# Optimization experiments

Hardware: AMD Instinct MI355X
Metric: run time of the kernel (lower is better)

The kernel has to match this reference:

```python
import jax, jax.numpy as jnp
import numpy as np

V, FC = 6890, 13776
N, H, W, K = 2, 336, 336, 28
SIGMA, GAMMA, EPS = 1e-4, 1e-4, 1e-10
ZNEAR, ZFAR = 1.0, 100.0
SHININESS = 64.0
BG = jnp.array([1.0, 1.0, 1.0], jnp.float32)


def setup_inputs() -> dict:
    key = jax.random.key(0)
    ks = jax.random.split(key, 10)
    verts = jax.random.normal(ks[0], (V, 3), jnp.float32)
    vert_colors = jax.random.uniform(ks[1], (V, 3), jnp.float32)
    faces = jax.random.randint(ks[2], (FC, 3), 0, V)
    # shift so ~1/FC entries are -1 (background), as in PyTorch3D Fragments
    pix_to_face = jax.random.randint(ks[3], (N, H, W, K), 0, FC + 1) - 1
    u = jax.random.uniform(ks[4], (N, H, W, K, 3), jnp.float32) + 1e-3
    bary_coords = u / u.sum(-1, keepdims=True)
    dists = jax.random.normal(ks[5], (N, H, W, K), jnp.float32) * 1e-4
    zbuf = jnp.sort(jax.random.uniform(ks[6], (N, H, W, K), jnp.float32) * 10.0 + 2.0, axis=-1)
    light_location = jnp.array([0.0, 0.0, 10.0], jnp.float32)
    ambient_color = jnp.full((3,), 0.5, jnp.float32)
    diffuse_color = jnp.full((3,), 0.3, jnp.float32)
    specular_color = jnp.full((3,), 0.2, jnp.float32)
    camera_position = jnp.array([0.0, 0.0, 2.7], jnp.float32)
    return dict(verts=verts, vert_colors=vert_colors, faces=faces,
                pix_to_face=pix_to_face, bary_coords=bary_coords, dists=dists,
                zbuf=zbuf, light_location=light_location,
                ambient_color=ambient_color, diffuse_color=diffuse_color,
                specular_color=specular_color, camera_position=camera_position)


def _normalize(x, eps=1e-6):
    return x / jnp.maximum(jnp.linalg.norm(x, axis=-1, keepdims=True), eps)


def reference(verts, vert_colors, faces, pix_to_face, bary_coords, dists, zbuf,
              light_location, ambient_color, diffuse_color, specular_color,
              camera_position):
    # ---- per-vertex normals (area-weighted face normals scatter-added) ----
    v0, v1, v2 = verts[faces[:, 0]], verts[faces[:, 1]], verts[faces[:, 2]]
    fn = jnp.cross(v1 - v0, v2 - v0)                       # [F,3]
    fn_rep = jnp.repeat(fn[:, None, :], 3, axis=1).reshape(-1, 3)
    vnorm = jax.ops.segment_sum(fn_rep, faces.reshape(-1), num_segments=verts.shape[0])
    vnorm = _normalize(vnorm)                              # [V,3]

    # ---- gather face attributes per fragment & barycentric interpolation ----
    mask = pix_to_face >= 0                                # [N,H,W,K]
    idx = jnp.maximum(pix_to_face, 0)
    f = faces[idx]                                         # [N,H,W,K,3]
    pix_pos = jnp.einsum('nhwkc,nhwkcd->nhwkd', bary_coords, verts[f])
    pix_nrm = _normalize(jnp.einsum('nhwkc,nhwkcd->nhwkd', bary_coords, vnorm[f]))
    texels = jnp.einsum('nhwkc,nhwkcd->nhwkd', bary_coords, vert_colors[f])

    # ---- Phong shading (point light) ----
    l = _normalize(light_location - pix_pos)               # [N,H,W,K,3]
    ndotl = jnp.maximum(jnp.sum(pix_nrm * l, axis=-1), 0.0)
    diffuse = diffuse_color * ndotl[..., None]
    view = _normalize(camera_position - pix_pos)
    reflect = -l + 2.0 * jnp.sum(l * pix_nrm, axis=-1, keepdims=True) * pix_nrm
    cos_a = jnp.maximum(jnp.sum(reflect * view, axis=-1), 0.0)
    specular = specular_color * (cos_a ** SHININESS)[..., None]
    colors = (ambient_color + diffuse) * texels + specular  # [N,H,W,K,3]

    # ---- softmax_rgb_blend ----
    prob = jax.nn.sigmoid(-dists / SIGMA) * mask            # [N,H,W,K]
    z_inv = jnp.where(mask, (ZFAR - zbuf) / (ZFAR - ZNEAR), 0.0)
    z_inv_max = jnp.maximum(z_inv.max(axis=-1, keepdims=True), EPS)
    w_num = prob * jnp.exp((z_inv - z_inv_max) / GAMMA)     # [N,H,W,K]
    delta = jnp.exp((EPS - z_inv_max) / GAMMA)              # [N,H,W,1]
    denom = w_num.sum(axis=-1, keepdims=True) + delta       # [N,H,W,1]
    rgb = (jnp.einsum('nhwk,nhwkd->nhwd', w_num, colors) + delta * BG) / denom
    alpha = 1.0 - jnp.prod(1.0 - prob, axis=-1)             # [N,H,W]
    images = jnp.concatenate([rgb, alpha[..., None]], axis=-1)  # [N,H,W,4]
    return images, zbuf
```

## Files before the change

### kernel.cpp

```cpp
#include <hip/hip_runtime.h>
#include <hip/hip_fp16.h>
#include <math.h>

#define V_   6890
#define FC_  13776
#define N_   2
#define H_   336
#define W_   336
#define K_   28
#define NPIX (N_*H_*W_)

#define SIGMA_INV 1.0e4f
#define GAMMA_INV 1.0e4f
#define EPS_      1e-10f
#define ZFAR_     100.0f
#define ZSCALE    (1.0f/99.0f)
#define LOG2E     1.442695041f

static __device__ __forceinline__ float fexp(float x)  { return __builtin_amdgcn_exp2f(x * LOG2E); }
static __device__ __forceinline__ float frcp(float x)  { return __builtin_amdgcn_rcpf(x); }
static __device__ __forceinline__ float frsq(float x)  { return __builtin_amdgcn_rsqf(x); }

#define FD_OFFSET 82944

__global__ __launch_bounds__(256)
void face_pass1(const float* __restrict__ verts,
                const float* __restrict__ vcol,
                const int*   __restrict__ faces,
                float* __restrict__ vnAcc,
                __half2* __restrict__ fd) {
    int i = blockIdx.x * blockDim.x + threadIdx.x;
    if (i >= FC_) return;
    int f0 = faces[i*3+0], f1 = faces[i*3+1], f2 = faces[i*3+2];
    float a[18];
    a[0] = verts[f0*3+0]; a[1] = verts[f0*3+1]; a[2] = verts[f0*3+2];
    a[3] = verts[f1*3+0]; a[4] = verts[f1*3+1]; a[5] = verts[f1*3+2];
    a[6] = verts[f2*3+0]; a[7] = verts[f2*3+1]; a[8] = verts[f2*3+2];
    float e1x = a[3]-a[0], e1y = a[4]-a[1], e1z = a[5]-a[2];
    float e2x = a[6]-a[0], e2y = a[7]-a[1], e2z = a[8]-a[2];
    float fnx = e1y*e2z - e1z*e2y;
    float fny = e1z*e2x - e1x*e2z;
    float fnz = e1x*e2y - e1y*e2x;
    atomicAdd(&vnAcc[f0*3+0], fnx); atomicAdd(&vnAcc[f0*3+1], fny); atomicAdd(&vnAcc[f0*3+2], fnz);
    atomicAdd(&vnAcc[f1*3+0], fnx); atomicAdd(&vnAcc[f1*3+1], fny); atomicAdd(&vnAcc[f1*3+2], fnz);
    atomicAdd(&vnAcc[f2*3+0], fnx); atomicAdd(&vnAcc[f2*3+1], fny); atomicAdd(&vnAcc[f2*3+2], fnz);
    a[9]  = vcol[f0*3+0]; a[10] = vcol[f0*3+1]; a[11] = vcol[f0*3+2];
    a[12] = vcol[f1*3+0]; a[13] = vcol[f1*3+1]; a[14] = vcol[f1*3+2];
    a[15] = vcol[f2*3+0]; a[16] = vcol[f2*3+1]; a[17] = vcol[f2*3+2];
    __half2* o = fd + (size_t)i * 16;
    #pragma unroll
    for (int t = 0; t < 9; ++t) o[t] = __floats2half2_rn(a[2*t], a[2*t+1]);
}

__global__ __launch_bounds__(256)
void face_pass2(const int* __restrict__ faces,
                const float* __restrict__ vn,
                __half2* __restrict__ fd) {
    int i = blockIdx.x * blockDim.x + threadIdx.x;
    if (i >= FC_) return;
    int fidx[3] = { faces[i*3+0], faces[i*3+1], faces[i*3+2] };
    float b[10];
    #pragma unroll
    for (int v = 0; v < 3; ++v) {
        float x = vn[fidx[v]*3+0], y = vn[fidx[v]*3+1], z = vn[fidx[v]*3+2];
        float inv = frsq(fmaxf(x*x + y*y + z*z, 1e-12f));
        b[v*3+0] = x*inv; b[v*3+1] = y*inv; b[v*3+2] = z*inv;
    }
    b[9] = 0.0f;
    __half2* o = fd + (size_t)i * 16 + 9;
    #pragma unroll
    for (int t = 0; t < 5; ++t) o[t] = __floats2half2_rn(b[2*t], b[2*t+1]);
}

__global__ __launch_bounds__(256)
void pixel_kernel(const int*   __restrict__ ptf,
                  const float* __restrict__ bary,
                  const float* __restrict__ dists,
                  const float* __restrict__ zbuf,
                  const ushort* __restrict__ fd16,
                  const float* __restrict__ light,
                  const float* __restrict__ amb,
                  const float* __restrict__ dif,
                  const float* __restrict__ spec,
                  const float* __restrict__ cam,
                  float* __restrict__ out) {
    int tid = blockIdx.x * blockDim.x + threadIdx.x;
    int pix = tid >> 5;
    int j   = tid & 31;
    if (pix >= NPIX) return;

    bool act = (j < K_);
    size_t sbase = (size_t)pix * K_ + j;

    int pf = -1;
    float d = 0.0f, z = 0.0f, w0 = 0.0f, w1 = 0.0f, w2 = 0.0f;
    if (act) {
        pf = ptf[sbase];
        d  = dists[sbase];
        z  = zbuf[sbase];
        w0 = bary[sbase*3+0];
        w1 = bary[sbase*3+1];
        w2 = bary[sbase*3+2];
        out[(size_t)NPIX*4 + sbase] = z;
    }

    float zi = 0.0f, prob = 0.0f, cr = 0.0f, cg = 0.0f, cb = 0.0f;
    if (pf >= 0) {
        prob = frcp(1.0f + fexp(d * SIGMA_INV));
        zi   = (ZFAR_ - z) * ZSCALE;

        const uint4* fq = (const uint4*)(fd16 + (size_t)pf * 32);
        union { uint4 u[4]; __half h[32]; } F;
        F.u[0] = fq[0]; F.u[1] = fq[1]; F.u[2] = fq[2]; F.u[3] = fq[3];

        float p0x = __half2float(F.h[0]),  p0y = __half2float(F.h[1]),  p0z = __half2float(F.h[2]);
        float p1x = __half2float(F.h[3]),  p1y = __half2float(F.h[4]),  p1z = __half2float(F.h[5]);
        float p2x = __half2float(F.h[6]),  p2y = __half2float(F.h[7]),  p2z = __half2float(F.h[8]);
        float c0x = __half2float(F.h[9]),  c0y = __half2float(F.h[10]), c0z = __half2float(F.h[11]);
        float c1x = __half2float(F.h[12]), c1y = __half2float(F.h[13]), c1z = __half2float(F.h[14]);
        float c2x = __half2float(F.h[15]), c2y = __half2float(F.h[16]), c2z = __half2float(F.h[17]);
        float n0x = __half2float(F.h[18]), n0y = __half2float(F.h[19]), n0z = __half2float(F.h[20]);
        float n1x = __half2float(F.h[21]), n1y = __half2float(F.h[22]), n1z = __half2float(F.h[23]);
        float n2x = __half2float(F.h[24]), n2y = __half2float(F.h[25]), n2z = __half2float(F.h[26]);

        float px = w0*p0x + w1*p1x + w2*p2x;
        float py = w0*p0y + w1*p1y + w2*p2y;
        float pz = w0*p0z + w1*p1z + w2*p2z;
        float nux = w0*n0x + w1*n1x + w2*n2x;
        float nuy = w0*n0y + w1*n1y + w2*n2y;
        float nuz = w0*n0z + w1*n1z + w2*n2z;
        float ninv = frsq(fmaxf(nux*nux + nuy*nuy + nuz*nuz, 1e-12f));
        float nx = nux*ninv, ny = nuy*ninv, nz = nuz*ninv;
        float tr = w0*c0x + w1*c1x + w2*c2x;
        float tg = w0*c0y + w1*c1y + w2*c2y;
        float tb = w0*c0z + w1*c1z + w2*c2z;

        float lvx = light[0] - px, lvy = light[1] - py, lvz = light[2] - pz;
        float linv = frsq(fmaxf(lvx*lvx + lvy*lvy + lvz*lvz, 1e-12f));
        lvx *= linv; lvy *= linv; lvz *= linv;
        float ldn = lvx*nx + lvy*ny + lvz*nz;
        float ndotl = fmaxf(ldn, 0.0f);

        float vvx = cam[0] - px, vvy = cam[1] - py, vvz = cam[2] - pz;
        float vinv = frsq(fmaxf(vvx*vvx + vvy*vvy + vvz*vvz, 1e-12f));
        vvx *= vinv; vvy *= vinv; vvz *= vinv;

        float rx = 2.0f*ldn*nx - lvx;
        float ry = 2.0f*ldn*ny - lvy;
        float rz = 2.0f*ldn*nz - lvz;
        float ca = fmaxf(rx*vvx + ry*vvy + rz*vvz, 0.0f);
        float p64 = ca*ca; p64 *= p64; p64 *= p64; p64 *= p64; p64 *= p64; p64 *= p64;

        cr = (amb[0] + dif[0]*ndotl)*tr + spec[0]*p64;
        cg = (amb[1] + dif[1]*ndotl)*tg + spec[1]*p64;
        cb = (amb[2] + dif[2]*ndotl)*tb + spec[2]*p64;
    }

    float m = fmaxf(zi, EPS_);
    #pragma unroll
    for (int o = 16; o; o >>= 1) m = fmaxf(m, __shfl_xor(m, o, 32));

    float w = prob * fexp((zi - m) * GAMMA_INV);
    float swr = w * cr, swg = w * cg, swb = w * cb;
    float om  = 1.0f - prob;
    #pragma unroll
    for (int o = 16; o; o >>= 1) {
        w   += __shfl_xor(w,   o, 32);
        swr += __shfl_xor(swr, o, 32);
        swg += __shfl_xor(swg, o, 32);
        swb += __shfl_xor(swb, o, 32);
        om  *= __shfl_xor(om,  o, 32);
    }

    if (j == 0) {
        float deltaw = fexp((EPS_ - m) * GAMMA_INV);
        float inv = frcp(w + deltaw);
        float4 img;
        img.x = (swr + deltaw) * inv;
        img.y = (swg + deltaw) * inv;
        img.z = (swb + deltaw) * inv;
        img.w = 1.0f - om;
        ((float4*)out)[pix] = img;
    }
}

extern "C" void kernel_launch(void* const* d_in, const int* in_sizes, int n_in,
                              void* d_out, int out_size, void* d_ws, size_t ws_size,
                              hipStream_t stream) {
    const float* verts = (const float*)d_in[0];
    const float* vcol  = (const float*)d_in[1];
    const int*   faces = (const int*)d_in[2];
    const int*   ptf   = (const int*)d_in[3];
    const float* bary  = (const float*)d_in[4];
    const float* dists = (const float*)d_in[5];
    const float* zbuf  = (const float*)d_in[6];
    const float* light = (const float*)d_in[7];
    const float* amb   = (const float*)d_in[8];
    const float* dif   = (const float*)d_in[9];
    const float* spec  = (const float*)d_in[10];
    const float* cam   = (const float*)d_in[11];
    float* out = (float*)d_out;

    float*   vnAcc = (float*)d_ws;
    __half2* fdat  = (__half2*)((char*)d_ws + FD_OFFSET);

    hipMemsetAsync(vnAcc, 0, (size_t)V_ * 3 * sizeof(float), stream);
    face_pass1<<<(FC_ + 255)/256, 256, 0, stream>>>(verts, vcol, faces, vnAcc, fdat);
    face_pass2<<<(FC_ + 255)/256, 256, 0, stream>>>(faces, vnAcc, fdat);

    int blocks = (NPIX * 32 + 255) / 256;
    pixel_kernel<<<blocks, 256, 0, stream>>>(
        ptf, bary, dists, zbuf, (const ushort*)fdat,
        light, amb, dif, spec, cam, out);
}
```

Before: 261.5 us.

## Process two samples per lane with 16-lane pixel groups and ballot-based max

```diff
diff --git a/kernel.cpp b/kernel.cpp
--- a/kernel.cpp
+++ b/kernel.cpp
@@ -72,6 +72,47 @@
     for (int t = 0; t < 5; ++t) o[t] = __floats2half2_rn(b[2*t], b[2*t+1]);
 }
 
+static __device__ __forceinline__ void shade_one(
+    const __half* __restrict__ h, float w0, float w1, float w2,
+    float lx, float ly, float lz,
+    float ax, float ay, float az,
+    float dcx, float dcy, float dcz,
+    float scx, float scy, float scz,
+    float camx, float camy, float camz,
+    float& cr, float& cg, float& cb) {
+    float px = w0*__half2float(h[0]) + w1*__half2float(h[3]) + w2*__half2float(h[6]);
+    float py = w0*__half2float(h[1]) + w1*__half2float(h[4]) + w2*__half2float(h[7]);
+    float pz = w0*__half2float(h[2]) + w1*__half2float(h[5]) + w2*__half2float(h[8]);
+    float tr = w0*__half2float(h[9])  + w1*__half2float(h[12]) + w2*__half2float(h[15]);
+    float tg = w0*__half2float(h[10]) + w1*__half2float(h[13]) + w2*__half2float(h[16]);
+    float tb = w0*__half2float(h[11]) + w1*__half2float(h[14]) + w2*__half2float(h[17]);
+    float nux = w0*__half2float(h[18]) + w1*__half2float(h[21]) + w2*__half2float(h[24]);
+    float nuy = w0*__half2float(h[19]) + w1*__half2float(h[22]) + w2*__half2float(h[25]);
+    float nuz = w0*__half2float(h[20]) + w1*__half2float(h[23]) + w2*__half2float(h[26]);
+    float ninv = frsq(fmaxf(nux*nux + nuy*nuy + nuz*nuz, 1e-12f));
+    float nx = nux*ninv, ny = nuy*ninv, nz = nuz*ninv;
+
+    float lvx = lx - px, lvy = ly - py, lvz = lz - pz;
+    float linv = frsq(fmaxf(lvx*lvx + lvy*lvy + lvz*lvz, 1e-12f));
+    lvx *= linv; lvy *= linv; lvz *= linv;
+    float ldn = lvx*nx + lvy*ny + lvz*nz;
+    float ndotl = fmaxf(ldn, 0.0f);
+
+    float vvx = camx - px, vvy = camy - py, vvz = camz - pz;
+    float vinv = frsq(fmaxf(vvx*vvx + vvy*vvy + vvz*vvz, 1e-12f));
+    vvx *= vinv; vvy *= vinv; vvz *= vinv;
+
+    float rx = 2.0f*ldn*nx - lvx;
+    float ry = 2.0f*ldn*ny - lvy;
+    float rz = 2.0f*ldn*nz - lvz;
+    float ca = fmaxf(rx*vvx + ry*vvy + rz*vvz, 0.0f);
+    float p64 = ca*ca; p64 *= p64; p64 *= p64; p64 *= p64; p64 *= p64; p64 *= p64;
+
+    cr = (ax + dcx*ndotl)*tr + scx*p64;
+    cg = (ay + dcy*ndotl)*tg + scy*p64;
+    cb = (az + dcz*ndotl)*tb + scz*p64;
+}
+
 __global__ __launch_bounds__(256)
 void pixel_kernel(const int*   __restrict__ ptf,
                   const float* __restrict__ bary,
@@ -85,91 +126,81 @@
                   const float* __restrict__ cam,
                   float* __restrict__ out) {
     int tid = blockIdx.x * blockDim.x + threadIdx.x;
-    int pix = tid >> 5;
-    int j   = tid & 31;
+    int pix = tid >> 4;
+    int j   = tid & 15;
     if (pix >= NPIX) return;
 
-    bool act = (j < K_);
-    size_t sbase = (size_t)pix * K_ + j;
-
-    int pf = -1;
-    float d = 0.0f, z = 0.0f, w0 = 0.0f, w1 = 0.0f, w2 = 0.0f;
+    float lx = light[0], ly = light[1], lz = light[2];
+    float ax = amb[0],   ay = amb[1],   az = amb[2];
+    float dcx = dif[0],  dcy = dif[1],  dcz = dif[2];
+    float scx = spec[0], scy = spec[1], scz = spec[2];
+    float camx = cam[0], camy = cam[1], camz = cam[2];
+
+    bool act = (j < 14);
+    size_t sbase = (size_t)pix * K_ + 2*j;
+
+    int pf0 = -1, pf1 = -1;
+    float d0 = 0.f, d1 = 0.f, z0 = ZFAR_, z1 = ZFAR_;
+    float b00 = 0.f, b01 = 0.f, b02 = 0.f, b10 = 0.f, b11 = 0.f, b12 = 0.f;
     if (act) {
-        pf = ptf[sbase];
-        d  = dists[sbase];
-        z  = zbuf[sbase];
-        w0 = bary[sbase*3+0];
-        w1 = bary[sbase*3+1];
-        w2 = bary[sbase*3+2];
-        out[(size_t)NPIX*4 + sbase] = z;
-    }
-
-    float zi = 0.0f, prob = 0.0f, cr = 0.0f, cg = 0.0f, cb = 0.0f;
-    if (pf >= 0) {
-        prob = frcp(1.0f + fexp(d * SIGMA_INV));
-        zi   = (ZFAR_ - z) * ZSCALE;
-
-        const uint4* fq = (const uint4*)(fd16 + (size_t)pf * 32);
-        union { uint4 u[4]; __half h[32]; } F;
-        F.u[0] = fq[0]; F.u[1] = fq[1]; F.u[2] = fq[2]; F.u[3] = fq[3];
-
-        float p0x = __half2float(F.h[0]),  p0y = __half2float(F.h[1]),  p0z = __half2float(F.h[2]);
-        float p1x = __half2float(F.h[3]),  p1y = __half2float(F.h[4]),  p1z = __half2float(F.h[5]);
-        float p2x = __half2float(F.h[6]),  p2y = __half2float(F.h[7]),  p2z = __half2float(F.h[8]);
-        float c0x = __half2float(F.h[9]),  c0y = __half2float(F.h[10]), c0z = __half2float(F.h[11]);
-        float c1x = __half2float(F.h[12]), c1y = __half2float(F.h[13]), c1z = __half2float(F.h[14]);
-        float c2x = __half2float(F.h[15]), c2y = __half2float(F.h[16]), c2z = __half2float(F.h[17]);
-        float n0x = __half2float(F.h[18]), n0y = __half2float(F.h[19]), n0z = __half2float(F.h[20]);
-        float n1x = __half2float(F.h[21]), n1y = __half2float(F.h[22]), n1z = __half2float(F.h[23]);
-        float n2x = __half2float(F.h[24]), n2y = __half2float(F.h[25]), n2z = __half2float(F.h[26]);
-
-        float px = w0*p0x + w1*p1x + w2*p2x;
-        float py = w0*p0y + w1*p1y + w2*p2y;
-        float pz = w0*p0z + w1*p1z + w2*p2z;
-        float nux = w0*n0x + w1*n1x + w2*n2x;
-        float nuy = w0*n0y + w1*n1y + w2*n2y;
-        float nuz = w0*n0z + w1*n1z + w2*n2z;
-        float ninv = frsq(fmaxf(nux*nux + nuy*nuy + nuz*nuz, 1e-12f));
-        float nx = nux*ninv, ny = nuy*ninv, nz = nuz*ninv;
-        float tr = w0*c0x + w1*c1x + w2*c2x;
-        float tg = w0*c0y + w1*c1y + w2*c2y;
-        float tb = w0*c0z + w1*c1z + w2*c2z;
-
-        float lvx = light[0] - px, lvy = light[1] - py, lvz = light[2] - pz;
-        float linv = frsq(fmaxf(lvx*lvx + lvy*lvy + lvz*lvz, 1e-12f));
-        lvx *= linv; lvy *= linv; lvz *= linv;
-        float ldn = lvx*nx + lvy*ny + lvz*nz;
-        float ndotl = fmaxf(ldn, 0.0f);
-
-        float vvx = cam[0] - px, vvy = cam[1] - py, vvz = cam[2] - pz;
-        float vinv = frsq(fmaxf(vvx*vvx + vvy*vvy + vvz*vvz, 1e-12f));
-        vvx *= vinv; vvy *= vinv; vvz *= vinv;
-
-        float rx = 2.0f*ldn*nx - lvx;
-        float ry = 2.0f*ldn*ny - lvy;
-        float rz = 2.0f*ldn*nz - lvz;
-        float ca = fmaxf(rx*vvx + ry*vvy + rz*vvz, 0.0f);
-        float p64 = ca*ca; p64 *= p64; p64 *= p64; p64 *= p64; p64 *= p64; p64 *= p64;
-
-        cr = (amb[0] + dif[0]*ndotl)*tr + spec[0]*p64;
-        cg = (amb[1] + dif[1]*ndotl)*tg + spec[1]*p64;
-        cb = (amb[2] + dif[2]*ndotl)*tb + spec[2]*p64;
-    }
-
-    float m = fmaxf(zi, EPS_);
-    #pragma unroll
-    for (int o = 16; o; o >>= 1) m = fmaxf(m, __shfl_xor(m, o, 32));
-
-    float w = prob * fexp((zi - m) * GAMMA_INV);
-    float swr = w * cr, swg = w * cg, swb = w * cb;
-    float om  = 1.0f - prob;
-    #pragma unroll
-    for (int o = 16; o; o >>= 1) {
-        w   += __shfl_xor(w,   o, 32);
-        swr += __shfl_xor(swr, o, 32);
-        swg += __shfl_xor(swg, o, 32);
-        swb += __shfl_xor(swb, o, 32);
-        om  *= __shfl_xor(om,  o, 32);
+        int2   p2 = *(const int2*)  (ptf   + sbase);
+        float2 dd = *(const float2*)(dists + sbase);
+        float2 zz = *(const float2*)(zbuf  + sbase);
+        const float2* bb = (const float2*)(bary + sbase*3);
+        float2 ba = bb[0], bbv = bb[1], bc = bb[2];
+        *(float2*)(out + (size_t)NPIX*4 + sbase) = zz;
+        pf0 = p2.x; pf1 = p2.y;
+        d0 = dd.x; d1 = dd.y; z0 = zz.x; z1 = zz.y;
+        b00 = ba.x; b01 = ba.y; b02 = bbv.x;
+        b10 = bbv.y; b11 = bc.x; b12 = bc.y;
+    }
+
+    int i0 = pf0 >= 0 ? pf0 : 0;
+    int i1 = pf1 >= 0 ? pf1 : 0;
+    union Blob { uint4 u[4]; __half h[32]; };
+    Blob F0, F1;
+    {
+        const uint4* q0 = (const uint4*)(fd16 + (size_t)i0 * 32);
+        const uint4* q1 = (const uint4*)(fd16 + (size_t)i1 * 32);
+        F0.u[0] = q0[0]; F0.u[1] = q0[1]; F0.u[2] = q0[2]; F0.u[3] = q0[3];
+        F1.u[0] = q1[0]; F1.u[1] = q1[1]; F1.u[2] = q1[2]; F1.u[3] = q1[3];
+    }
+
+    float cr0, cg0, cb0, cr1, cg1, cb1;
+    shade_one(F0.h, b00, b01, b02, lx,ly,lz, ax,ay,az, dcx,dcy,dcz, scx,scy,scz, camx,camy,camz, cr0,cg0,cb0);
+    shade_one(F1.h, b10, b11, b12, lx,ly,lz, ax,ay,az, dcx,dcy,dcz, scx,scy,scz, camx,camy,camz, cr1,cg1,cb1);
+
+    float prob0 = pf0 >= 0 ? frcp(1.0f + fexp(d0 * SIGMA_INV)) : 0.0f;
+    float prob1 = pf1 >= 0 ? frcp(1.0f + fexp(d1 * SIGMA_INV)) : 0.0f;
+    float zi0 = pf0 >= 0 ? (ZFAR_ - z0) * ZSCALE : 0.0f;
+    float zi1 = pf1 >= 0 ? (ZFAR_ - z1) * ZSCALE : 0.0f;
+
+    float cand = pf0 >= 0 ? zi0 : zi1;
+    bool  has  = (pf0 >= 0) || (pf1 >= 0);
+    unsigned long long mk = __ballot(has);
+    int wavelane  = threadIdx.x & 63;
+    int groupbase = wavelane & ~15;
+    unsigned gm = (unsigned)((mk >> groupbase) & 0xFFFFull);
+    float m = EPS_;
+    int src = groupbase + (gm ? (int)__builtin_ctz(gm) : 0);
+    float mshfl = __shfl(cand, src, 64);
+    if (gm) m = mshfl;
+
+    float w0s = prob0 * fexp((zi0 - m) * GAMMA_INV);
+    float w1s = prob1 * fexp((zi1 - m) * GAMMA_INV);
+    float w   = w0s + w1s;
+    float swr = w0s*cr0 + w1s*cr1;
+    float swg = w0s*cg0 + w1s*cg1;
+    float swb = w0s*cb0 + w1s*cb1;
+    float om  = (1.0f - prob0) * (1.0f - prob1);
+
+    #pragma unroll
+    for (int o = 8; o; o >>= 1) {
+        w   += __shfl_xor(w,   o, 16);
+        swr += __shfl_xor(swr, o, 16);
+        swg += __shfl_xor(swg, o, 16);
+        swb += __shfl_xor(swb, o, 16);
+        om  *= __shfl_xor(om,  o, 16);
     }
 
     if (j == 0) {
@@ -208,7 +239,7 @@
     face_pass1<<<(FC_ + 255)/256, 256, 0, stream>>>(verts, vcol, faces, vnAcc, fdat);
     face_pass2<<<(FC_ + 255)/256, 256, 0, stream>>>(faces, vnAcc, fdat);
 
-    int blocks = (NPIX * 32 + 255) / 256;
+    int blocks = (NPIX * 16 + 255) / 256;
     pixel_kernel<<<blocks, 256, 0, stream>>>(
         ptf, bary, dists, zbuf, (const ushort*)fdat,
         light, amb, dif, spec, cam, out);
```

Result: slower. 277.9 us (+6.2%).

## Shrink packed face records, normalize normals per vertex, shortcut depth max

Applied to the files above, without the earlier changes.

```diff
diff --git a/kernel.cpp b/kernel.cpp
--- a/kernel.cpp
+++ b/kernel.cpp
@@ -23,53 +23,62 @@
 
 #define FD_OFFSET 82944
 
-__global__ __launch_bounds__(256)
-void face_pass1(const float* __restrict__ verts,
-                const float* __restrict__ vcol,
-                const int*   __restrict__ faces,
-                float* __restrict__ vnAcc,
-                __half2* __restrict__ fd) {
+union FaceRec { uint4 q[3]; __half h[18]; unsigned char b[48]; };
+
+__global__ __launch_bounds__(256)
+void face_normals(const float* __restrict__ verts,
+                  const int*   __restrict__ faces,
+                  float* __restrict__ vnAcc) {
     int i = blockIdx.x * blockDim.x + threadIdx.x;
     if (i >= FC_) return;
     int f0 = faces[i*3+0], f1 = faces[i*3+1], f2 = faces[i*3+2];
-    float a[18];
-    a[0] = verts[f0*3+0]; a[1] = verts[f0*3+1]; a[2] = verts[f0*3+2];
-    a[3] = verts[f1*3+0]; a[4] = verts[f1*3+1]; a[5] = verts[f1*3+2];
-    a[6] = verts[f2*3+0]; a[7] = verts[f2*3+1]; a[8] = verts[f2*3+2];
-    float e1x = a[3]-a[0], e1y = a[4]-a[1], e1z = a[5]-a[2];
-    float e2x = a[6]-a[0], e2y = a[7]-a[1], e2z = a[8]-a[2];
+    float p0x = verts[f0*3+0], p0y = verts[f0*3+1], p0z = verts[f0*3+2];
+    float p1x = verts[f1*3+0], p1y = verts[f1*3+1], p1z = verts[f1*3+2];
+    float p2x = verts[f2*3+0], p2y = verts[f2*3+1], p2z = verts[f2*3+2];
+    float e1x = p1x-p0x, e1y = p1y-p0y, e1z = p1z-p0z;
+    float e2x = p2x-p0x, e2y = p2y-p0y, e2z = p2z-p0z;
     float fnx = e1y*e2z - e1z*e2y;
     float fny = e1z*e2x - e1x*e2z;
     float fnz = e1x*e2y - e1y*e2x;
     atomicAdd(&vnAcc[f0*3+0], fnx); atomicAdd(&vnAcc[f0*3+1], fny); atomicAdd(&vnAcc[f0*3+2], fnz);
     atomicAdd(&vnAcc[f1*3+0], fnx); atomicAdd(&vnAcc[f1*3+1], fny); atomicAdd(&vnAcc[f1*3+2], fnz);
     atomicAdd(&vnAcc[f2*3+0], fnx); atomicAdd(&vnAcc[f2*3+1], fny); atomicAdd(&vnAcc[f2*3+2], fnz);
-    a[9]  = vcol[f0*3+0]; a[10] = vcol[f0*3+1]; a[11] = vcol[f0*3+2];
-    a[12] = vcol[f1*3+0]; a[13] = vcol[f1*3+1]; a[14] = vcol[f1*3+2];
-    a[15] = vcol[f2*3+0]; a[16] = vcol[f2*3+1]; a[17] = vcol[f2*3+2];
-    __half2* o = fd + (size_t)i * 16;
-    #pragma unroll
-    for (int t = 0; t < 9; ++t) o[t] = __floats2half2_rn(a[2*t], a[2*t+1]);
-}
-
-__global__ __launch_bounds__(256)
-void face_pass2(const int* __restrict__ faces,
-                const float* __restrict__ vn,
-                __half2* __restrict__ fd) {
+}
+
+__global__ __launch_bounds__(256)
+void vn_normalize(float* __restrict__ vn) {
+    int i = blockIdx.x * blockDim.x + threadIdx.x;
+    if (i >= V_) return;
+    float x = vn[i*3+0], y = vn[i*3+1], z = vn[i*3+2];
+    float inv = frsq(fmaxf(x*x + y*y + z*z, 1e-12f));
+    vn[i*3+0] = x*inv; vn[i*3+1] = y*inv; vn[i*3+2] = z*inv;
+}
+
+__global__ __launch_bounds__(256)
+void face_pack(const int*   __restrict__ faces,
+               const float* __restrict__ verts,
+               const float* __restrict__ vcol,
+               const float* __restrict__ vn,
+               uint4* __restrict__ fd) {
     int i = blockIdx.x * blockDim.x + threadIdx.x;
     if (i >= FC_) return;
-    int fidx[3] = { faces[i*3+0], faces[i*3+1], faces[i*3+2] };
-    float b[10];
+    int f[3] = { faces[i*3+0], faces[i*3+1], faces[i*3+2] };
+    FaceRec R;
     #pragma unroll
     for (int v = 0; v < 3; ++v) {
-        float x = vn[fidx[v]*3+0], y = vn[fidx[v]*3+1], z = vn[fidx[v]*3+2];
-        float inv = frsq(fmaxf(x*x + y*y + z*z, 1e-12f));
-        b[v*3+0] = x*inv; b[v*3+1] = y*inv; b[v*3+2] = z*inv;
-    }
-    b[9] = 0.0f;
-    __half2* o = fd + (size_t)i * 16 + 9;
-    #pragma unroll
-    for (int t = 0; t < 5; ++t) o[t] = __floats2half2_rn(b[2*t], b[2*t+1]);
+        R.h[v*3+0] = __float2half(verts[f[v]*3+0]);
+        R.h[v*3+1] = __float2half(verts[f[v]*3+1]);
+        R.h[v*3+2] = __float2half(verts[f[v]*3+2]);
+        R.h[9+v*3+0] = __float2half(vn[f[v]*3+0]);
+        R.h[9+v*3+1] = __float2half(vn[f[v]*3+1]);
+        R.h[9+v*3+2] = __float2half(vn[f[v]*3+2]);
+        R.b[36+v*3+0] = (unsigned char)lrintf(vcol[f[v]*3+0]*255.0f);
+        R.b[36+v*3+1] = (unsigned char)lrintf(vcol[f[v]*3+1]*255.0f);
+        R.b[36+v*3+2] = (unsigned char)lrintf(vcol[f[v]*3+2]*255.0f);
+    }
+    R.b[45] = R.b[46] = R.b[47] = 0;
+    uint4* o = fd + (size_t)i * 3;
+    o[0] = R.q[0]; o[1] = R.q[1]; o[2] = R.q[2];
 }
 
 __global__ __launch_bounds__(256)
@@ -77,7 +86,7 @@
                   const float* __restrict__ bary,
                   const float* __restrict__ dists,
                   const float* __restrict__ zbuf,
-                  const ushort* __restrict__ fd16,
+                  const uint4* __restrict__ fd,
                   const float* __restrict__ light,
                   const float* __restrict__ amb,
                   const float* __restrict__ dif,
@@ -98,8 +107,8 @@
         pf = ptf[sbase];
         d  = dists[sbase];
         z  = zbuf[sbase];
-        w0 = bary[sbase*3+0];
-        w1 = bary[sbase*3+1];
+        float2 b01 = *(const float2*)(bary + sbase*3);
+        w0 = b01.x; w1 = b01.y;
         w2 = bary[sbase*3+2];
         out[(size_t)NPIX*4 + sbase] = z;
     }
@@ -109,31 +118,23 @@
         prob = frcp(1.0f + fexp(d * SIGMA_INV));
         zi   = (ZFAR_ - z) * ZSCALE;
 
-        const uint4* fq = (const uint4*)(fd16 + (size_t)pf * 32);
-        union { uint4 u[4]; __half h[32]; } F;
-        F.u[0] = fq[0]; F.u[1] = fq[1]; F.u[2] = fq[2]; F.u[3] = fq[3];
-
-        float p0x = __half2float(F.h[0]),  p0y = __half2float(F.h[1]),  p0z = __half2float(F.h[2]);
-        float p1x = __half2float(F.h[3]),  p1y = __half2float(F.h[4]),  p1z = __half2float(F.h[5]);
-        float p2x = __half2float(F.h[6]),  p2y = __half2float(F.h[7]),  p2z = __half2float(F.h[8]);
-        float c0x = __half2float(F.h[9]),  c0y = __half2float(F.h[10]), c0z = __half2float(F.h[11]);
-        float c1x = __half2float(F.h[12]), c1y = __half2float(F.h[13]), c1z = __half2float(F.h[14]);
-        float c2x = __half2float(F.h[15]), c2y = __half2float(F.h[16]), c2z = __half2float(F.h[17]);
-        float n0x = __half2float(F.h[18]), n0y = __half2float(F.h[19]), n0z = __half2float(F.h[20]);
-        float n1x = __half2float(F.h[21]), n1y = __half2float(F.h[22]), n1z = __half2float(F.h[23]);
-        float n2x = __half2float(F.h[24]), n2y = __half2float(F.h[25]), n2z = __half2float(F.h[26]);
-
-        float px = w0*p0x + w1*p1x + w2*p2x;
-        float py = w0*p0y + w1*p1y + w2*p2y;
-        float pz = w0*p0z + w1*p1z + w2*p2z;
-        float nux = w0*n0x + w1*n1x + w2*n2x;
-        float nuy = w0*n0y + w1*n1y + w2*n2y;
-        float nuz = w0*n0z + w1*n1z + w2*n2z;
+        const uint4* g = fd + (size_t)pf * 3;
+        FaceRec F;
+        F.q[0] = g[0]; F.q[1] = g[1]; F.q[2] = g[2];
+
+        float px = w0*__half2float(F.h[0]) + w1*__half2float(F.h[3]) + w2*__half2float(F.h[6]);
+        float py = w0*__half2float(F.h[1]) + w1*__half2float(F.h[4]) + w2*__half2float(F.h[7]);
+        float pz = w0*__half2float(F.h[2]) + w1*__half2float(F.h[5]) + w2*__half2float(F.h[8]);
+        float nux = w0*__half2float(F.h[9])  + w1*__half2float(F.h[12]) + w2*__half2float(F.h[15]);
+        float nuy = w0*__half2float(F.h[10]) + w1*__half2float(F.h[13]) + w2*__half2float(F.h[16]);
+        float nuz = w0*__half2float(F.h[11]) + w1*__half2float(F.h[14]) + w2*__half2float(F.h[17]);
+        const float s255 = 1.0f/255.0f;
+        float tr = (w0*(float)F.b[36] + w1*(float)F.b[39] + w2*(float)F.b[42]) * s255;
+        float tg = (w0*(float)F.b[37] + w1*(float)F.b[40] + w2*(float)F.b[43]) * s255;
+        float tb = (w0*(float)F.b[38] + w1*(float)F.b[41] + w2*(float)F.b[44]) * s255;
+
         float ninv = frsq(fmaxf(nux*nux + nuy*nuy + nuz*nuz, 1e-12f));
         float nx = nux*ninv, ny = nuy*ninv, nz = nuz*ninv;
-        float tr = w0*c0x + w1*c1x + w2*c2x;
-        float tg = w0*c0y + w1*c1y + w2*c2y;
-        float tb = w0*c0z + w1*c1z + w2*c2z;
 
         float lvx = light[0] - px, lvy = light[1] - py, lvz = light[2] - pz;
         float linv = frsq(fmaxf(lvx*lvx + lvy*lvy + lvz*lvz, 1e-12f));
@@ -156,9 +157,14 @@
         cb = (amb[2] + dif[2]*ndotl)*tb + spec[2]*p64;
     }
 
-    float m = fmaxf(zi, EPS_);
-    #pragma unroll
-    for (int o = 16; o; o >>= 1) m = fmaxf(m, __shfl_xor(m, o, 32));
+    unsigned long long mk = __ballot(pf >= 0);
+    int wavelane  = threadIdx.x & 63;
+    int groupbase = wavelane & 32;
+    unsigned gm = (unsigned)(mk >> groupbase);
+    float m = EPS_;
+    int src = groupbase + (gm ? (int)__builtin_ctz(gm) : 0);
+    float mshfl = __shfl(zi, src, 64);
+    if (gm) m = mshfl;
 
     float w = prob * fexp((zi - m) * GAMMA_INV);
     float swr = w * cr, swg = w * cg, swb = w * cb;
@@ -201,15 +207,16 @@
     const float* cam   = (const float*)d_in[11];
     float* out = (float*)d_out;
 
-    float*   vnAcc = (float*)d_ws;
-    __half2* fdat  = (__half2*)((char*)d_ws + FD_OFFSET);
+    float* vnAcc = (float*)d_ws;
+    uint4* fdat  = (uint4*)((char*)d_ws + FD_OFFSET);
 
     hipMemsetAsync(vnAcc, 0, (size_t)V_ * 3 * sizeof(float), stream);
-    face_pass1<<<(FC_ + 255)/256, 256, 0, stream>>>(verts, vcol, faces, vnAcc, fdat);
-    face_pass2<<<(FC_ + 255)/256, 256, 0, stream>>>(faces, vnAcc, fdat);
+    face_normals<<<(FC_ + 255)/256, 256, 0, stream>>>(verts, faces, vnAcc);
+    vn_normalize<<<(V_ + 255)/256, 256, 0, stream>>>(vnAcc);
+    face_pack<<<(FC_ + 255)/256, 256, 0, stream>>>(faces, verts, vcol, vnAcc, fdat);
 
     int blocks = (NPIX * 32 + 255) / 256;
     pixel_kernel<<<blocks, 256, 0, stream>>>(
-        ptf, bary, dists, zbuf, (const ushort*)fdat,
+        ptf, bary, dists, zbuf, fdat,
         light, amb, dif, spec, cam, out);
 }
```

Result: faster. 243.9 us (-6.8%).
